# Optimization experiments

Measured on AMD Instinct MI355X. Metric: run time of the kernel, lower is better.

## Reference

```python
import jax, jax.numpy as jnp
import numpy as np

LN_EPS = 1e-5


def setup_inputs() -> dict:
    key = jax.random.key(0)
    ks = jax.random.split(key, 4)
    B, D, N = 256, 1024, 100000
    scale = 1.0 / np.sqrt(D)
    return {
        "query": jax.random.normal(ks[0], (B, D), dtype=jnp.float32),
        "W1": jax.random.normal(ks[1], (D, D), dtype=jnp.float32) * scale,
        "b1": jnp.zeros((D,), dtype=jnp.float32),
        "ln_g": jnp.ones((D,), dtype=jnp.float32),
        "ln_b": jnp.zeros((D,), dtype=jnp.float32),
        "W2": jax.random.normal(ks[2], (D, D), dtype=jnp.float32) * scale,
        "b2": jnp.zeros((D,), dtype=jnp.float32),
        "memory": jax.random.normal(ks[3], (N, D), dtype=jnp.float32),
        "k": 16,
    }


def _l2norm(x):
    # F.normalize(p=2, dim=-1): x / max(||x||, eps) with eps=1e-12
    n = jnp.sqrt(jnp.sum(x * x, axis=-1, keepdims=True))
    return x / jnp.maximum(n, 1e-12)


def _layernorm(x, g, b):
    mu = jnp.mean(x, axis=-1, keepdims=True)
    var = jnp.mean((x - mu) ** 2, axis=-1, keepdims=True)
    return (x - mu) * jax.lax.rsqrt(var + LN_EPS) * g + b


def reference(query, W1, b1, ln_g, ln_b, W2, b2, memory, k):
    # project(): Linear -> LayerNorm -> GELU (exact) -> Linear -> L2 normalize
    h = query @ W1.T + b1                      # [B, D]
    h = _layernorm(h, ln_g, ln_b)
    h = jax.nn.gelu(h, approximate=False)
    refined = _l2norm(h @ W2.T + b2)           # [B, D]

    # retrieve_similar(): cosine sims against normalized memory bank, then top-k
    mem_n = _l2norm(memory)                    # [N, D]
    sims = refined @ mem_n.T                   # [B, N]
    topk_vals, topk_idx = jax.lax.top_k(sims, k)   # [B, k]
    retrieved = mem_n[topk_idx]                # [B, k, D] gather
    return refined, topk_vals, topk_idx, retrieved
```

## Files before the change

kernel.cpp:

```cpp
#include <hip/hip_runtime.h>
#include <float.h>
#include <math.h>

#define D 1024
#define BQ 256
#define NMEM 100000
#define TOPK 16
#define NT_TOT 1563
#define SIMS_BLOCKS 1024

typedef __attribute__((ext_vector_type(4))) float f32x4;
typedef __attribute__((ext_vector_type(8))) short s16x8;

__device__ __forceinline__ void mfma16(f32x4& d, s16x8 a, s16x8 b) {
  asm("v_mfma_f32_16x16x32_bf16 %0, %1, %2, %0" : "+v"(d) : "v"(a), "v"(b));
}

__device__ __forceinline__ unsigned short bf16rtne(float x) {
  unsigned u = __float_as_uint(x);
  unsigned r = u + 0x7fffu + ((u >> 16) & 1u);
  return (unsigned short)(r >> 16);
}

__device__ __forceinline__ void cvt8(float4 a, float4 b, s16x8* hi, s16x8* lo,
                                     float* ssq) {
  float xs[8] = {a.x, a.y, a.z, a.w, b.x, b.y, b.z, b.w};
  union { s16x8 v; unsigned short u[8]; } H, L;
#pragma unroll
  for (int e = 0; e < 8; ++e) {
    float x = xs[e];
    unsigned short h = bf16rtne(x);
    float hf = __uint_as_float(((unsigned)h) << 16);
    H.u[e] = (short)h;
    L.u[e] = (short)bf16rtne(x - hf);
    *ssq = fmaf(x, x, *ssq);
  }
  *hi = H.v;
  *lo = L.v;
}


__device__ __forceinline__ float waveReduceSum(float v) {
#pragma unroll
  for (int o = 32; o > 0; o >>= 1) v += __shfl_xor(v, o, 64);
  return v;
}

__device__ __forceinline__ float blockReduceSum(float v, float* sbuf) {
  v = waveReduceSum(v);
  int w = threadIdx.x >> 6;
  if ((threadIdx.x & 63) == 0) sbuf[w] = v;
  __syncthreads();
  float r = sbuf[0] + sbuf[1] + sbuf[2] + sbuf[3];
  __syncthreads();
  return r;
}


__global__ __launch_bounds__(256) void prep_bf16_kernel(
    const float* __restrict__ src, float* __restrict__ dst, int R16) {
  int g = blockIdx.x * 256 + threadIdx.x;
  int l = g & 63;
  int mt = (g >> 6) % R16;
  int kb = (g >> 6) / R16;
  int row = mt * 16 + (l & 15);
  int k0 = kb * 32 + ((l >> 4) << 3);
  const float* s = src + (size_t)row * D + k0;
  float4 v0 = *(const float4*)s;
  float4 v1 = *(const float4*)(s + 4);
  float xs[8] = {v0.x, v0.y, v0.z, v0.w, v1.x, v1.y, v1.z, v1.w};
  union { uint4 q; unsigned short u[8]; } H, L;
#pragma unroll
  for (int e = 0; e < 8; ++e) {
    float x = xs[e];
    unsigned short h = bf16rtne(x);
    float hf = __uint_as_float(((unsigned)h) << 16);
    H.u[e] = h;
    L.u[e] = bf16rtne(x - hf);
  }
  char* db = (char*)dst + (size_t)kb * (R16 * 2048) + mt * 2048 + l * 16;
  *(uint4*)db = H.q;
  *(uint4*)(db + 1024) = L.q;
}


__global__ __launch_bounds__(256) void mfma_gemm_kernel(
    const float* __restrict__ Afr, const float* __restrict__ Wfr,
    float* __restrict__ part) {
  int t = threadIdx.x;
  int w = t >> 6, l = t & 63;
  int ct = blockIdx.x & 63;
  int kc = blockIdx.x >> 6;
  f32x4 acc[4];
  f32x4 zz = {0.f, 0.f, 0.f, 0.f};
#pragma unroll
  for (int mi = 0; mi < 4; ++mi) acc[mi] = zz;
  const char* ab0 = (const char*)Afr + w * 8192 + l * 16;
  const char* bb0 = (const char*)Wfr + ct * 2048 + l * 16;
#pragma unroll 2
  for (int s = 0; s < 8; ++s) {
    int kb = kc * 8 + s;
    const char* bb = bb0 + (size_t)kb * 131072;
    s16x8 bh = *(const s16x8*)(bb);
    s16x8 bl = *(const s16x8*)(bb + 1024);
    const char* ab = ab0 + (size_t)kb * 32768;
#pragma unroll
    for (int mi = 0; mi < 4; ++mi) {
      s16x8 ah = *(const s16x8*)(ab + mi * 2048);
      s16x8 al = *(const s16x8*)(ab + mi * 2048 + 1024);
      mfma16(acc[mi], ah, bh);
      mfma16(acc[mi], ah, bl);
      mfma16(acc[mi], al, bh);
    }
  }
  float* pb = part + (size_t)kc * 262144 + ct * 16 + (l & 15);
#pragma unroll
  for (int mi = 0; mi < 4; ++mi)
#pragma unroll
    for (int j = 0; j < 4; ++j) {
      int row = w * 64 + mi * 16 + ((l >> 4) << 2) + j;
      pb[(size_t)row * 1024] = acc[mi][j];
    }
}


__global__ __launch_bounds__(256) void reduce_ln_gelu_kernel(
    const float* __restrict__ part, const float* __restrict__ bias,
    const float* __restrict__ g, const float* __restrict__ b,
    float* __restrict__ Hf) {
  __shared__ float sbuf[4];
  int row = blockIdx.x, t = threadIdx.x;
  const float* p = part + (size_t)row * 1024 + t * 4;
  float4 x0 = *(const float4*)(p);
  float4 x1 = *(const float4*)(p + 262144);
  float4 x2 = *(const float4*)(p + 524288);
  float4 x3 = *(const float4*)(p + 786432);
  float4 bb = *(const float4*)(bias + t * 4);
  float vx = x0.x + x1.x + x2.x + x3.x + bb.x;
  float vy = x0.y + x1.y + x2.y + x3.y + bb.y;
  float vz = x0.z + x1.z + x2.z + x3.z + bb.z;
  float vw = x0.w + x1.w + x2.w + x3.w + bb.w;
  float s = blockReduceSum(vx + vy + vz + vw, sbuf);
  float mu = s * (1.0f / D);
  float dx = vx - mu, dy = vy - mu, dz = vz - mu, dw = vw - mu;
  float ss = blockReduceSum(dx * dx + dy * dy + dz * dz + dw * dw, sbuf);
  float rstd = rsqrtf(ss * (1.0f / D) + 1e-5f);
  float4 gg = *(const float4*)(g + t * 4);
  float4 be = *(const float4*)(b + t * 4);
  float y[4];
  y[0] = dx * rstd * gg.x + be.x;
  y[1] = dy * rstd * gg.y + be.y;
  y[2] = dz * rstd * gg.z + be.z;
  y[3] = dw * rstd * gg.w + be.w;
  const float c = 0.70710678118654752f;
  union { uint2 q; unsigned short u[4]; } H, L;
#pragma unroll
  for (int e = 0; e < 4; ++e) {
    float ye = 0.5f * y[e] * (1.0f + erff(y[e] * c));
    unsigned short h = bf16rtne(ye);
    float hf = __uint_as_float(((unsigned)h) << 16);
    H.u[e] = h;
    L.u[e] = bf16rtne(ye - hf);
  }
  int kb = t >> 3, oct = (t >> 1) & 3;
  char* db = (char*)Hf + (size_t)kb * 32768 + (row >> 4) * 2048 +
             ((row & 15) + oct * 16) * 16 + (t & 1) * 8;
  *(uint2*)db = H.q;
  *(uint2*)(db + 1024) = L.q;
}


__global__ __launch_bounds__(256) void reduce_l2norm_kernel(
    const float* __restrict__ part, const float* __restrict__ bias,
    float* __restrict__ outRef, float* __restrict__ Af) {
  __shared__ float sbuf[4];
  int row = blockIdx.x, t = threadIdx.x;
  const float* p = part + (size_t)row * 1024 + t * 4;
  float4 x0 = *(const float4*)(p);
  float4 x1 = *(const float4*)(p + 262144);
  float4 x2 = *(const float4*)(p + 524288);
  float4 x3 = *(const float4*)(p + 786432);
  float4 bb = *(const float4*)(bias + t * 4);
  float vx = x0.x + x1.x + x2.x + x3.x + bb.x;
  float vy = x0.y + x1.y + x2.y + x3.y + bb.y;
  float vz = x0.z + x1.z + x2.z + x3.z + bb.z;
  float vw = x0.w + x1.w + x2.w + x3.w + bb.w;
  float ss = blockReduceSum(vx * vx + vy * vy + vz * vz + vw * vw, sbuf);
  float inv = 1.0f / fmaxf(sqrtf(ss), 1e-12f);
  float y[4] = {vx * inv, vy * inv, vz * inv, vw * inv};
  *(float4*)(outRef + (size_t)row * D + t * 4) =
      make_float4(y[0], y[1], y[2], y[3]);
  union { uint2 q; unsigned short u[4]; } H, L;
#pragma unroll
  for (int e = 0; e < 4; ++e) {
    unsigned short h = bf16rtne(y[e]);
    float hf = __uint_as_float(((unsigned)h) << 16);
    H.u[e] = h;
    L.u[e] = bf16rtne(y[e] - hf);
  }
  int kb = t >> 3, oct = (t >> 1) & 3;
  char* db = (char*)Af + (size_t)kb * 32768 + (row >> 4) * 2048 +
             ((row & 15) + oct * 16) * 16 + (t & 1) * 8;
  *(uint2*)db = H.q;
  *(uint2*)(db + 1024) = L.q;
}

__global__ void zero_ctrs_kernel(int* c) { c[threadIdx.x] = 0; }


#define SBODY(J, BP, ACh, ACl, ANh, ANl, RC0, RC1, RP0, RP1, DOPFB, DOPFA,    \
              DOCONV)                                                          \
  do {                                                                         \
    if (DOCONV) {                                                              \
      s16x8 bhn_, bln_;                                                        \
      cvt8(RC0, RC1, &bhn_, &bln_, &ssq);                                      \
      char* bw_ = smem + (1 - (BP)) * 8192 + bwoff;                            \
      *(s16x8*)bw_ = bhn_;                                                     \
      *(s16x8*)(bw_ + 1024) = bln_;                                            \
    }                                                                          \
    if (DOPFA) {                                                               \
      const char* an_ = afbytes + (size_t)((J) + 1) * 32768 + w4x + l * 16;    \
      _Pragma("unroll") for (int mi = 0; mi < 4; ++mi) {                       \
        ANh[mi] = *(const s16x8*)(an_ + mi * 2048);                            \
        ANl[mi] = *(const s16x8*)(an_ + mi * 2048 + 1024);                     \
      }                                                                        \
    }                                                                          \
    if (DOPFB) {                                                               \
      const float* p_ = bsrc + ((J) + 3) * 32;                                 \
      RP0 = *(const float4*)p_;                                                \
      RP1 = *(const float4*)(p_ + 4);                                          \
    }                                                                          \
    __builtin_amdgcn_s_setprio(1);                                             \
    _Pragma("unroll") for (int ni = 0; ni < 4; ++ni) {                         \
      const char* bb_ = smem + (BP)*8192 + ni * 2048 + l * 16;                 \
      s16x8 bh_ = *(const s16x8*)bb_;                                          \
      s16x8 bl_ = *(const s16x8*)(bb_ + 1024);                                 \
      _Pragma("unroll") for (int mi = 0; mi < 4; ++mi) {                       \
        mfma16(acc[mi][ni], ACh[mi], bh_);                                     \
        mfma16(acc[mi][ni], ACh[mi], bl_);                                     \
        mfma16(acc[mi][ni], ACl[mi], bh_);                                     \
      }                                                                        \
    }                                                                          \
    __builtin_amdgcn_s_setprio(0);                                             \
    asm volatile("s_waitcnt lgkmcnt(0)\n\ts_barrier" ::: "memory");            \
    __builtin_amdgcn_sched_barrier(0);                                         \
  } while (0)

__global__ __launch_bounds__(256, 2) void sims_gemm_kernel(
    const float* __restrict__ Afrag, const float* __restrict__ mem,
    float* __restrict__ invn, int* __restrict__ ctr,
    float* __restrict__ simsbuf, int ntiles, int chunk_n0, int stride_cols) {
  __shared__ __align__(16) char smem[16384];
  __shared__ float sInvF[64];
  __shared__ int s_tile;
  const int t = threadIdx.x;
  const int w = t >> 6, l = t & 63;
  const int w4x = (w * 4) * 2048;
  const int brow_loc = t >> 2;
  const int kseg = t & 3;
  const int bwoff = (brow_loc >> 4) * 2048 + ((brow_loc & 15) + kseg * 16) * 16;
  const char* afbytes = (const char*)Afrag;

  while (true) {
    if (t == 0) s_tile = atomicAdd(ctr, 1);
    __syncthreads();
    const int unit = s_tile;
    __syncthreads();
    if (unit >= ntiles) break;
    const int n0 = chunk_n0 + unit * 64;
    const int brow = min(n0 + brow_loc, NMEM - 1);
    const float* bsrc = mem + (size_t)brow * D + kseg * 8;

    f32x4 acc[4][4];
    f32x4 zz = {0.f, 0.f, 0.f, 0.f};
#pragma unroll
    for (int mi = 0; mi < 4; ++mi)
#pragma unroll
      for (int ni = 0; ni < 4; ++ni) acc[mi][ni] = zz;
    float ssq = 0.f;

    float4 r0a, r0b, r1a, r1b, r2a, r2b;
    s16x8 s0h[4], s0l[4], s1h[4], s1l[4];

    r0a = *(const float4*)bsrc;
    r0b = *(const float4*)(bsrc + 4);
    r1a = *(const float4*)(bsrc + 32);
    r1b = *(const float4*)(bsrc + 36);
    r2a = *(const float4*)(bsrc + 64);
    r2b = *(const float4*)(bsrc + 68);
    {
      const char* a0_ = afbytes + w4x + l * 16;
#pragma unroll
      for (int mi = 0; mi < 4; ++mi) {
        s0h[mi] = *(const s16x8*)(a0_ + mi * 2048);
        s0l[mi] = *(const s16x8*)(a0_ + mi * 2048 + 1024);
      }
    }
    {
      s16x8 bh0, bl0;
      cvt8(r0a, r0b, &bh0, &bl0, &ssq);
      *(s16x8*)(smem + bwoff) = bh0;
      *(s16x8*)(smem + bwoff + 1024) = bl0;
    }
    asm volatile("s_waitcnt lgkmcnt(0)\n\ts_barrier" ::: "memory");
    __builtin_amdgcn_sched_barrier(0);

#pragma unroll 1
    for (int jb = 0; jb < 24; jb += 6) {
      SBODY(jb + 0, 0, s0h, s0l, s1h, s1l, r1a, r1b, r0a, r0b, 1, 1, 1);
      SBODY(jb + 1, 1, s1h, s1l, s0h, s0l, r2a, r2b, r1a, r1b, 1, 1, 1);
      SBODY(jb + 2, 0, s0h, s0l, s1h, s1l, r0a, r0b, r2a, r2b, 1, 1, 1);
      SBODY(jb + 3, 1, s1h, s1l, s0h, s0l, r1a, r1b, r0a, r0b, 1, 1, 1);
      SBODY(jb + 4, 0, s0h, s0l, s1h, s1l, r2a, r2b, r1a, r1b, 1, 1, 1);
      SBODY(jb + 5, 1, s1h, s1l, s0h, s0l, r0a, r0b, r2a, r2b, 1, 1, 1);
    }
    SBODY(24, 0, s0h, s0l, s1h, s1l, r1a, r1b, r0a, r0b, 1, 1, 1);
    SBODY(25, 1, s1h, s1l, s0h, s0l, r2a, r2b, r1a, r1b, 1, 1, 1);
    SBODY(26, 0, s0h, s0l, s1h, s1l, r0a, r0b, r2a, r2b, 1, 1, 1);
    SBODY(27, 1, s1h, s1l, s0h, s0l, r1a, r1b, r0a, r0b, 1, 1, 1);
    SBODY(28, 0, s0h, s0l, s1h, s1l, r2a, r2b, r1a, r1b, 1, 1, 1);
    SBODY(29, 1, s1h, s1l, s0h, s0l, r0a, r0b, r2a, r2b, 0, 1, 1);
    SBODY(30, 0, s0h, s0l, s1h, s1l, r1a, r1b, r0a, r0b, 0, 1, 1);
    SBODY(31, 1, s1h, s1l, s0h, s0l, r2a, r2b, r1a, r1b, 0, 0, 0);

    float s2 = ssq + __shfl_xor(ssq, 1, 64);
    s2 = s2 + __shfl_xor(s2, 2, 64);
    float inv = 1.0f / fmaxf(sqrtf(s2), 1e-12f);
    if (kseg == 0) {
      sInvF[brow_loc] = inv;
      int col = n0 + brow_loc;
      if (col < NMEM) invn[col] = inv;
    }
    __syncthreads();
    float siv[4];
#pragma unroll
    for (int ni = 0; ni < 4; ++ni) siv[ni] = sInvF[ni * 16 + (l & 15)];
    float* srow = simsbuf + (size_t)(unit * 64);
#pragma unroll
    for (int mi = 0; mi < 4; ++mi)
#pragma unroll
      for (int jj = 0; jj < 4; ++jj) {
        int row = w * 64 + mi * 16 + ((l >> 4) << 2) + jj;
        float* rp = srow + (size_t)row * stride_cols;
#pragma unroll
        for (int ni = 0; ni < 4; ++ni)
          rp[ni * 16 + (l & 15)] = acc[mi][ni][jj] * siv[ni];
      }
    __syncthreads();
  }
}


__global__ __launch_bounds__(512) void topk_chunk_kernel(
    const float* __restrict__ simsbuf, int stride_cols, int chunk_n0,
    int nvalid, int seglen, float* __restrict__ cv, int* __restrict__ ci) {
  __shared__ float wvv[8];
  __shared__ int wii[8];
  __shared__ float sbv;
  __shared__ int sbi;
  int row = blockIdx.x & 255;
  int seg = blockIdx.x >> 8;
  int c0beg = seg * seglen;
  int c0end = c0beg + seglen;
  if (c0end > nvalid) c0end = nvalid;
  int t = threadIdx.x;
  const float* S = simsbuf + (size_t)row * stride_cols;
  float tv[16];
  int ti[16];
#pragma unroll
  for (int s = 0; s < 16; ++s) { tv[s] = -FLT_MAX; ti[s] = 2147483647; }
  float curMin = -FLT_MAX;
  for (int c0 = c0beg + t * 4; c0 < c0end; c0 += 2048) {
    float vv[4] = {-FLT_MAX, -FLT_MAX, -FLT_MAX, -FLT_MAX};
    if (c0 + 4 <= c0end) {
      float4 v = *(const float4*)(S + c0);
      vv[0] = v.x; vv[1] = v.y; vv[2] = v.z; vv[3] = v.w;
    } else {
#pragma unroll
      for (int e = 0; e < 4; ++e)
        if (c0 + e < c0end) vv[e] = S[c0 + e];
    }
#pragma unroll
    for (int e = 0; e < 4; ++e) {
      float v = vv[e];
      if (v > curMin) {
        int n = chunk_n0 + c0 + e;
        int ms = 0;
        float mv = tv[0];
#pragma unroll
        for (int s = 1; s < 16; ++s)
          if (tv[s] < mv) { mv = tv[s]; ms = s; }
#pragma unroll
        for (int s = 0; s < 16; ++s)
          if (s == ms) { tv[s] = v; ti[s] = n; }
        curMin = tv[0];
#pragma unroll
        for (int s = 1; s < 16; ++s) curMin = fminf(curMin, tv[s]);
      }
    }
  }
  float lastV = FLT_MAX;
  int lastI = -1;
  for (int pass = 0; pass < TOPK; ++pass) {
    float bv = -FLT_MAX;
    int bi = 2147483647;
#pragma unroll
    for (int s = 0; s < 16; ++s) {
      float v = tv[s];
      int idx = ti[s];
      bool qual = (v < lastV) || (v == lastV && idx > lastI);
      bool bet = (v > bv) || (v == bv && idx < bi);
      if (qual && bet) { bv = v; bi = idx; }
    }
#pragma unroll
    for (int o = 32; o > 0; o >>= 1) {
      float v2 = __shfl_xor(bv, o, 64);
      int i2 = __shfl_xor(bi, o, 64);
      if (v2 > bv || (v2 == bv && i2 < bi)) { bv = v2; bi = i2; }
    }
    if ((t & 63) == 0) { wvv[t >> 6] = bv; wii[t >> 6] = bi; }
    __syncthreads();
    if (t == 0) {
      float fv = wvv[0];
      int fi = wii[0];
#pragma unroll
      for (int u = 1; u < 8; ++u) {
        if (wvv[u] > fv || (wvv[u] == fv && wii[u] < fi)) {
          fv = wvv[u];
          fi = wii[u];
        }
      }
      sbv = fv;
      sbi = fi;
      cv[seg * 4096 + row * TOPK + pass] = fv;
      ci[seg * 4096 + row * TOPK + pass] = fi;
    }
    __syncthreads();
    lastV = sbv;
    lastI = sbi;
  }
}


__global__ __launch_bounds__(64) void final_merge_kernel(
    const float* __restrict__ cand_v, const int* __restrict__ cand_i,
    int nlists, float* __restrict__ out_vals, float* __restrict__ out_idx) {
  int row = blockIdx.x, l = threadIdx.x;
  int nc = nlists * TOPK;
  float mv[8];
  int mi_[8];
#pragma unroll
  for (int u = 0; u < 8; ++u) {
    int p = l + u * 64;
    if (p < nc) {
      int ch = p >> 4;
      mv[u] = cand_v[ch * 4096 + row * TOPK + (p & 15)];
      mi_[u] = cand_i[ch * 4096 + row * TOPK + (p & 15)];
    } else {
      mv[u] = -FLT_MAX;
      mi_[u] = 2147483647;
    }
  }
  float lastV = FLT_MAX;
  int lastI = -1;
  for (int pass = 0; pass < TOPK; ++pass) {
    float bv = -FLT_MAX;
    int bi = 2147483647;
#pragma unroll
    for (int u = 0; u < 8; ++u) {
      bool qual = (mv[u] < lastV) || (mv[u] == lastV && mi_[u] > lastI);
      bool bet = (mv[u] > bv) || (mv[u] == bv && mi_[u] < bi);
      if (qual && bet) { bv = mv[u]; bi = mi_[u]; }
    }
#pragma unroll
    for (int o = 32; o > 0; o >>= 1) {
      float v2 = __shfl_xor(bv, o, 64);
      int i2 = __shfl_xor(bi, o, 64);
      if (v2 > bv || (v2 == bv && i2 < bi)) { bv = v2; bi = i2; }
    }
    bv = __shfl(bv, 0, 64);
    bi = __shfl(bi, 0, 64);
    if (l == 0) {
      out_vals[row * TOPK + pass] = bv;
      out_idx[row * TOPK + pass] = (float)bi;
    }
    lastV = bv;
    lastI = bi;
  }
}


__global__ __launch_bounds__(256) void gather_kernel(
    const float* __restrict__ out_idx, const float* __restrict__ mem,
    const float* __restrict__ invn, float* __restrict__ out_retr) {
  int p = blockIdx.x;
  int idx = (int)out_idx[p];
  float inv = invn[idx];
  int c = threadIdx.x * 4;
  float4 v = *(const float4*)(mem + (size_t)idx * D + c);
  v.x *= inv; v.y *= inv; v.z *= inv; v.w *= inv;
  *(float4*)(out_retr + (size_t)p * D + c) = v;
}


extern "C" void kernel_launch(void* const* d_in, const int* in_sizes, int n_in,
                              void* d_out, int out_size, void* d_ws,
                              size_t ws_size, hipStream_t stream) {
  const float* query = (const float*)d_in[0];
  const float* W1 = (const float*)d_in[1];
  const float* b1 = (const float*)d_in[2];
  const float* ln_g = (const float*)d_in[3];
  const float* ln_b = (const float*)d_in[4];
  const float* W2 = (const float*)d_in[5];
  const float* b2 = (const float*)d_in[6];
  const float* mem = (const float*)d_in[7];

  float* out = (float*)d_out;
  float* out_refined = out;
  float* out_vals = out + 262144;
  float* out_idx = out + 262144 + 4096;
  float* out_retr = out + 262144 + 8192;

  float* wsp = (float*)d_ws;
  float* invn = wsp;
  float* Qf = wsp + 100352;
  float* Af = wsp + 362496;
  float* W1f = wsp + 624640;
  float* W2f = wsp + 1673216;
  float* part = wsp + 2721792;
  float* cand_v = wsp + 3770368;
  int* cand_i = (int*)(wsp + 3901440);
  int* ctrs = (int*)(wsp + 4032512);
  float* sims = wsp + 4032576;

  long ws_floats = (long)(ws_size / 4);
  long avail = ws_floats - 4032640;
  int tpc = (int)(avail / 16384);
  if (tpc > NT_TOT) tpc = NT_TOT;
  if (tpc < 1) tpc = 1;
  int nchunk = (NT_TOT + tpc - 1) / tpc;
  if (nchunk > 32) nchunk = 32;
  tpc = (NT_TOT + nchunk - 1) / nchunk;
  int stride = tpc * 64;
  int nseg = (nchunk <= 8) ? 4 : 1;

  zero_ctrs_kernel<<<1, 64, 0, stream>>>(ctrs);
  prep_bf16_kernel<<<128, 256, 0, stream>>>(query, Qf, 16);
  prep_bf16_kernel<<<512, 256, 0, stream>>>(W1, W1f, 64);
  prep_bf16_kernel<<<512, 256, 0, stream>>>(W2, W2f, 64);
  mfma_gemm_kernel<<<256, 256, 0, stream>>>(Qf, W1f, part);
  reduce_ln_gelu_kernel<<<256, 256, 0, stream>>>(part, b1, ln_g, ln_b, Qf);
  mfma_gemm_kernel<<<256, 256, 0, stream>>>(Qf, W2f, part);
  reduce_l2norm_kernel<<<256, 256, 0, stream>>>(part, b2, out_refined, Af);
  for (int c = 0; c < nchunk; ++c) {
    int t0 = c * tpc;
    int nt = NT_TOT - t0;
    if (nt > tpc) nt = tpc;
    if (nt <= 0) break;
    int base = t0 * 64;
    sims_gemm_kernel<<<SIMS_BLOCKS, 256, 0, stream>>>(Af, mem, invn, ctrs + c,
                                                      sims, nt, base, stride);
    int nvalid = NMEM - base;
    if (nvalid > nt * 64) nvalid = nt * 64;
    int seglen = ((nvalid + nseg - 1) / nseg + 3) & ~3;
    topk_chunk_kernel<<<256 * nseg, 512, 0, stream>>>(
        sims, stride, base, nvalid, seglen, cand_v + c * nseg * 4096,
        cand_i + c * nseg * 4096);
  }
  final_merge_kernel<<<256, 64, 0, stream>>>(cand_v, cand_i, nchunk * nseg,
                                             out_vals, out_idx);
  gather_kernel<<<BQ * TOPK, 256, 0, stream>>>(out_idx, mem, invn, out_retr);
}
```

Baseline: 415.1 us.

## Use 512-thread blocks with 8 waves splitting query rows and swizzled LDS

The sims GEMM block grows from 4 to 8 waves, and each wave now covers 32 query rows instead of 64, which halves accumulators and A-fragment registers per thread. Memory-row loading changes to one float4 per thread across 8 k-quarters, and the LDS layout is XOR-swizzled to reduce bank conflicts on writes and reads. The grid goes from 1024 to 512 blocks. More waves per block are meant to hide latency better, at the cost of more per-block barriers and a different occupancy and register balance.

```diff
diff --git a/kernel.cpp b/kernel.cpp
--- a/kernel.cpp
+++ b/kernel.cpp
@@ -7,7 +7,7 @@
 #define NMEM 100000
 #define TOPK 16
 #define NT_TOT 1563
-#define SIMS_BLOCKS 1024
+#define SIMS_BLOCKS 512
 
 typedef __attribute__((ext_vector_type(4))) float f32x4;
 typedef __attribute__((ext_vector_type(8))) short s16x8;
@@ -22,21 +22,21 @@
   return (unsigned short)(r >> 16);
 }
 
-__device__ __forceinline__ void cvt8(float4 a, float4 b, s16x8* hi, s16x8* lo,
+__device__ __forceinline__ void cvt4(float4 a, uint2* hi, uint2* lo,
                                      float* ssq) {
-  float xs[8] = {a.x, a.y, a.z, a.w, b.x, b.y, b.z, b.w};
-  union { s16x8 v; unsigned short u[8]; } H, L;
-#pragma unroll
-  for (int e = 0; e < 8; ++e) {
+  float xs[4] = {a.x, a.y, a.z, a.w};
+  union { uint2 q; unsigned short u[4]; } H, L;
+#pragma unroll
+  for (int e = 0; e < 4; ++e) {
     float x = xs[e];
     unsigned short h = bf16rtne(x);
     float hf = __uint_as_float(((unsigned)h) << 16);
-    H.u[e] = (short)h;
-    L.u[e] = (short)bf16rtne(x - hf);
+    H.u[e] = h;
+    L.u[e] = bf16rtne(x - hf);
     *ssq = fmaf(x, x, *ssq);
   }
-  *hi = H.v;
-  *lo = L.v;
+  *hi = H.q;
+  *lo = L.q;
 }
 
 
@@ -208,34 +208,31 @@
 __global__ void zero_ctrs_kernel(int* c) { c[threadIdx.x] = 0; }
 
 
-#define SBODY(J, BP, ACh, ACl, ANh, ANl, RC0, RC1, RP0, RP1, DOPFB, DOPFA,    \
-              DOCONV)                                                          \
+#define SBODY(J, BP, ACh, ACl, ANh, ANl, RC, RN, DOPFB, DOPFA, DOCONV)        \
   do {                                                                         \
     if (DOCONV) {                                                              \
-      s16x8 bhn_, bln_;                                                        \
-      cvt8(RC0, RC1, &bhn_, &bln_, &ssq);                                      \
+      uint2 bh_, bl_;                                                          \
+      cvt4(RC, &bh_, &bl_, &ssq);                                              \
       char* bw_ = smem + (1 - (BP)) * 8192 + bwoff;                            \
-      *(s16x8*)bw_ = bhn_;                                                     \
-      *(s16x8*)(bw_ + 1024) = bln_;                                            \
+      *(uint2*)bw_ = bh_;                                                      \
+      *(uint2*)(bw_ + 1024) = bl_;                                             \
     }                                                                          \
     if (DOPFA) {                                                               \
-      const char* an_ = afbytes + (size_t)((J) + 1) * 32768 + w4x + l * 16;    \
-      _Pragma("unroll") for (int mi = 0; mi < 4; ++mi) {                       \
+      const char* an_ = afbytes + (size_t)((J) + 1) * 32768 + w2x + l * 16;    \
+      _Pragma("unroll") for (int mi = 0; mi < 2; ++mi) {                       \
         ANh[mi] = *(const s16x8*)(an_ + mi * 2048);                            \
         ANl[mi] = *(const s16x8*)(an_ + mi * 2048 + 1024);                     \
       }                                                                        \
     }                                                                          \
     if (DOPFB) {                                                               \
-      const float* p_ = bsrc + ((J) + 3) * 32;                                 \
-      RP0 = *(const float4*)p_;                                                \
-      RP1 = *(const float4*)(p_ + 4);                                          \
+      RN = *(const float4*)(bsrc + ((J) + 3) * 32);                            \
     }                                                                          \
     __builtin_amdgcn_s_setprio(1);                                             \
     _Pragma("unroll") for (int ni = 0; ni < 4; ++ni) {                         \
-      const char* bb_ = smem + (BP)*8192 + ni * 2048 + l * 16;                 \
+      const char* bb_ = smem + (BP)*8192 + ni * 2048 + lswz;                   \
       s16x8 bh_ = *(const s16x8*)bb_;                                          \
       s16x8 bl_ = *(const s16x8*)(bb_ + 1024);                                 \
-      _Pragma("unroll") for (int mi = 0; mi < 4; ++mi) {                       \
+      _Pragma("unroll") for (int mi = 0; mi < 2; ++mi) {                       \
         mfma16(acc[mi][ni], ACh[mi], bh_);                                     \
         mfma16(acc[mi][ni], ACh[mi], bl_);                                     \
         mfma16(acc[mi][ni], ACl[mi], bh_);                                     \
@@ -246,7 +243,7 @@
     __builtin_amdgcn_sched_barrier(0);                                         \
   } while (0)
 
-__global__ __launch_bounds__(256, 2) void sims_gemm_kernel(
+__global__ __launch_bounds__(512) void sims_gemm_kernel(
     const float* __restrict__ Afrag, const float* __restrict__ mem,
     float* __restrict__ invn, int* __restrict__ ctr,
     float* __restrict__ simsbuf, int ntiles, int chunk_n0, int stride_cols) {
@@ -255,10 +252,14 @@
   __shared__ int s_tile;
   const int t = threadIdx.x;
   const int w = t >> 6, l = t & 63;
-  const int w4x = (w * 4) * 2048;
-  const int brow_loc = t >> 2;
-  const int kseg = t & 3;
-  const int bwoff = (brow_loc >> 4) * 2048 + ((brow_loc & 15) + kseg * 16) * 16;
+  const int w2x = w * 4096;
+  const int brow_loc = t >> 3;
+  const int kq = t & 7;
+  const int koct = kq >> 1;
+  const int bwoff = (brow_loc >> 4) * 2048 +
+                    (((brow_loc & 15) ^ (koct << 2)) + koct * 16) * 16 +
+                    (kq & 1) * 8;
+  const int lswz = (((l & 15) ^ ((l >> 4) << 2)) + ((l >> 4) << 4)) * 16;
   const char* afbytes = (const char*)Afrag;
 
   while (true) {
@@ -269,64 +270,62 @@
     if (unit >= ntiles) break;
     const int n0 = chunk_n0 + unit * 64;
     const int brow = min(n0 + brow_loc, NMEM - 1);
-    const float* bsrc = mem + (size_t)brow * D + kseg * 8;
-
-    f32x4 acc[4][4];
+    const float* bsrc = mem + (size_t)brow * D + kq * 4;
+
+    f32x4 acc[2][4];
     f32x4 zz = {0.f, 0.f, 0.f, 0.f};
 #pragma unroll
-    for (int mi = 0; mi < 4; ++mi)
+    for (int mi = 0; mi < 2; ++mi)
 #pragma unroll
       for (int ni = 0; ni < 4; ++ni) acc[mi][ni] = zz;
     float ssq = 0.f;
 
-    float4 r0a, r0b, r1a, r1b, r2a, r2b;
-    s16x8 s0h[4], s0l[4], s1h[4], s1l[4];
-
-    r0a = *(const float4*)bsrc;
-    r0b = *(const float4*)(bsrc + 4);
-    r1a = *(const float4*)(bsrc + 32);
-    r1b = *(const float4*)(bsrc + 36);
-    r2a = *(const float4*)(bsrc + 64);
-    r2b = *(const float4*)(bsrc + 68);
+    float4 r0, r1, r2;
+    s16x8 s0h[2], s0l[2], s1h[2], s1l[2];
+
+    r0 = *(const float4*)bsrc;
+    r1 = *(const float4*)(bsrc + 32);
+    r2 = *(const float4*)(bsrc + 64);
     {
-      const char* a0_ = afbytes + w4x + l * 16;
-#pragma unroll
-      for (int mi = 0; mi < 4; ++mi) {
+      const char* a0_ = afbytes + w2x + l * 16;
+#pragma unroll
+      for (int mi = 0; mi < 2; ++mi) {
         s0h[mi] = *(const s16x8*)(a0_ + mi * 2048);
         s0l[mi] = *(const s16x8*)(a0_ + mi * 2048 + 1024);
       }
     }
     {
-      s16x8 bh0, bl0;
-      cvt8(r0a, r0b, &bh0, &bl0, &ssq);
-      *(s16x8*)(smem + bwoff) = bh0;
-      *(s16x8*)(smem + bwoff + 1024) = bl0;
+      uint2 bh0, bl0;
+      cvt4(r0, &bh0, &bl0, &ssq);
+      *(uint2*)(smem + bwoff) = bh0;
+      *(uint2*)(smem + bwoff + 1024) = bl0;
     }
     asm volatile("s_waitcnt lgkmcnt(0)\n\ts_barrier" ::: "memory");
     __builtin_amdgcn_sched_barrier(0);
 
 #pragma unroll 1
     for (int jb = 0; jb < 24; jb += 6) {
-      SBODY(jb + 0, 0, s0h, s0l, s1h, s1l, r1a, r1b, r0a, r0b, 1, 1, 1);
-      SBODY(jb + 1, 1, s1h, s1l, s0h, s0l, r2a, r2b, r1a, r1b, 1, 1, 1);
-      SBODY(jb + 2, 0, s0h, s0l, s1h, s1l, r0a, r0b, r2a, r2b, 1, 1, 1);
-      SBODY(jb + 3, 1, s1h, s1l, s0h, s0l, r1a, r1b, r0a, r0b, 1, 1, 1);
-      SBODY(jb + 4, 0, s0h, s0l, s1h, s1l, r2a, r2b, r1a, r1b, 1, 1, 1);
-      SBODY(jb + 5, 1, s1h, s1l, s0h, s0l, r0a, r0b, r2a, r2b, 1, 1, 1);
-    }
-    SBODY(24, 0, s0h, s0l, s1h, s1l, r1a, r1b, r0a, r0b, 1, 1, 1);
-    SBODY(25, 1, s1h, s1l, s0h, s0l, r2a, r2b, r1a, r1b, 1, 1, 1);
-    SBODY(26, 0, s0h, s0l, s1h, s1l, r0a, r0b, r2a, r2b, 1, 1, 1);
-    SBODY(27, 1, s1h, s1l, s0h, s0l, r1a, r1b, r0a, r0b, 1, 1, 1);
-    SBODY(28, 0, s0h, s0l, s1h, s1l, r2a, r2b, r1a, r1b, 1, 1, 1);
-    SBODY(29, 1, s1h, s1l, s0h, s0l, r0a, r0b, r2a, r2b, 0, 1, 1);
-    SBODY(30, 0, s0h, s0l, s1h, s1l, r1a, r1b, r0a, r0b, 0, 1, 1);
-    SBODY(31, 1, s1h, s1l, s0h, s0l, r2a, r2b, r1a, r1b, 0, 0, 0);
+      SBODY(jb + 0, 0, s0h, s0l, s1h, s1l, r1, r0, 1, 1, 1);
+      SBODY(jb + 1, 1, s1h, s1l, s0h, s0l, r2, r1, 1, 1, 1);
+      SBODY(jb + 2, 0, s0h, s0l, s1h, s1l, r0, r2, 1, 1, 1);
+      SBODY(jb + 3, 1, s1h, s1l, s0h, s0l, r1, r0, 1, 1, 1);
+      SBODY(jb + 4, 0, s0h, s0l, s1h, s1l, r2, r1, 1, 1, 1);
+      SBODY(jb + 5, 1, s1h, s1l, s0h, s0l, r0, r2, 1, 1, 1);
+    }
+    SBODY(24, 0, s0h, s0l, s1h, s1l, r1, r0, 1, 1, 1);
+    SBODY(25, 1, s1h, s1l, s0h, s0l, r2, r1, 1, 1, 1);
+    SBODY(26, 0, s0h, s0l, s1h, s1l, r0, r2, 1, 1, 1);
+    SBODY(27, 1, s1h, s1l, s0h, s0l, r1, r0, 1, 1, 1);
+    SBODY(28, 0, s0h, s0l, s1h, s1l, r2, r1, 1, 1, 1);
+    SBODY(29, 1, s1h, s1l, s0h, s0l, r0, r2, 0, 1, 1);
+    SBODY(30, 0, s0h, s0l, s1h, s1l, r1, r0, 0, 1, 1);
+    SBODY(31, 1, s1h, s1l, s0h, s0l, r2, r1, 0, 0, 0);
 
     float s2 = ssq + __shfl_xor(ssq, 1, 64);
     s2 = s2 + __shfl_xor(s2, 2, 64);
+    s2 = s2 + __shfl_xor(s2, 4, 64);
     float inv = 1.0f / fmaxf(sqrtf(s2), 1e-12f);
-    if (kseg == 0) {
+    if (kq == 0) {
       sInvF[brow_loc] = inv;
       int col = n0 + brow_loc;
       if (col < NMEM) invn[col] = inv;
@@ -337,10 +336,10 @@
     for (int ni = 0; ni < 4; ++ni) siv[ni] = sInvF[ni * 16 + (l & 15)];
     float* srow = simsbuf + (size_t)(unit * 64);
 #pragma unroll
-    for (int mi = 0; mi < 4; ++mi)
+    for (int mi = 0; mi < 2; ++mi)
 #pragma unroll
       for (int jj = 0; jj < 4; ++jj) {
-        int row = w * 64 + mi * 16 + ((l >> 4) << 2) + jj;
+        int row = w * 32 + mi * 16 + ((l >> 4) << 2) + jj;
         float* rp = srow + (size_t)row * stride_cols;
 #pragma unroll
         for (int ni = 0; ni < 4; ++ni)
@@ -558,7 +557,7 @@
     if (nt > tpc) nt = tpc;
     if (nt <= 0) break;
     int base = t0 * 64;
-    sims_gemm_kernel<<<SIMS_BLOCKS, 256, 0, stream>>>(Af, mem, invn, ctrs + c,
+    sims_gemm_kernel<<<SIMS_BLOCKS, 512, 0, stream>>>(Af, mem, invn, ctrs + c,
                                                       sims, nt, base, stride);
     int nvalid = NMEM - base;
     if (nvalid > nt * 64) nvalid = nt * 64;
```

After: 372.4 us. 10.3% less time.
